# Kernel tuning notes

Measured on AMD Instinct MI355X. Metric: run time of the kernel, lower is better.

The kernel has to match this reference:

```python
import jax, jax.numpy as jnp
import numpy as np

B, L, E, D, A = 32, 2048, 1024, 1024, 1024

def setup_inputs() -> dict:
    key = jax.random.key(0)
    k1, k2, k3, k4, k5 = jax.random.split(key, 5)
    s_e = 1.0 / np.sqrt(E)
    s_d = 1.0 / np.sqrt(D)
    s_a = 1.0 / np.sqrt(A)
    return {
        "encoder_outputs": jax.random.normal(k1, (B, L, E), dtype=jnp.float32),
        "decoder_hidden": jax.random.normal(k2, (B, D), dtype=jnp.float32),
        "mask": jnp.ones((B, L), dtype=jnp.int32),
        # nn.Linear weights are [out, in]; uniform(-1/sqrt(in), 1/sqrt(in))
        "W1": jax.random.uniform(k3, (A, E), jnp.float32, -s_e, s_e),
        "W2": jax.random.uniform(k4, (A, D), jnp.float32, -s_d, s_d),
        "v": jax.random.uniform(k5, (1, A), jnp.float32, -s_a, s_a),
    }

def reference(encoder_outputs, decoder_hidden, mask, W1, W2, v):
    # enc_t: [B,L,A], dec_t: [B,1,A]
    enc_t = jnp.einsum('ble,ae->bla', encoder_outputs, W1)
    dec_t = jnp.einsum('bd,ad->ba', decoder_hidden, W2)[:, None, :]
    combined = jnp.tanh(enc_t + dec_t)                       # [B,L,A]
    scores = jnp.einsum('bla,a->bl', combined, v[0])          # [B,L]
    scores = jnp.where(mask == 0, -jnp.inf, scores)
    attn = jax.nn.softmax(scores, axis=-1)                    # [B,L]
    context = jnp.einsum('bl,ble->be', attn, encoder_outputs) # [B,E]
    return (context, attn)
```

## Files before the change

kernel.cpp:

```cpp
#include <hip/hip_runtime.h>
#include <stdint.h>

typedef __bf16 bf16x8 __attribute__((ext_vector_type(8)));
typedef float f32x4 __attribute__((ext_vector_type(4)));
typedef unsigned short ushort8v __attribute__((ext_vector_type(8)));

__device__ __forceinline__ void gload_lds16(const void* g, void* l) {
  __builtin_amdgcn_global_load_lds(
      (const __attribute__((address_space(1))) void*)g,
      (__attribute__((address_space(3))) void*)l, 16, 0, 0);
}

__device__ __forceinline__ unsigned short f2bf(float f) {
  union { float f; unsigned int u; } x; x.f = f;
  unsigned int r = x.u + 0x7FFFu + ((x.u >> 16) & 1u);
  return (unsigned short)(r >> 16);
}

__device__ __forceinline__ float ftanh(float x) {
  float ax = fabsf(x);
  float e = __expf(-2.0f * ax);
  float r = (1.0f - e) / (1.0f + e);
  return copysignf(r, x);
}

__global__ __launch_bounds__(256) void w1cvt_kernel(
    const float* __restrict__ W1, unsigned short* __restrict__ w1b) {
  const int g = blockIdx.x * 256 + threadIdx.x;
  const int chunk = g >> 9;
  const int dpos = (g & 511) * 16;
  const int ntile = chunk >> 5, kstep = chunk & 31;
  const int col = dpos >> 6;
  const int k0 = (dpos & 63) >> 1;
  const float* src = W1 + (size_t)(ntile * 128 + col) * 1024 + kstep * 32 + k0;
  const float4 v0 = *(const float4*)src;
  const float4 v1 = *(const float4*)(src + 4);
  ushort8v o;
  o[0] = f2bf(v0.x); o[1] = f2bf(v0.y); o[2] = f2bf(v0.z); o[3] = f2bf(v0.w);
  o[4] = f2bf(v1.x); o[5] = f2bf(v1.y); o[6] = f2bf(v1.z); o[7] = f2bf(v1.w);
  *((ushort8v*)w1b + g) = o;
}

__global__ __launch_bounds__(256) void dec_proj_kernel(
    const float* __restrict__ dec, const float* __restrict__ W2,
    float* __restrict__ u) {
  __shared__ __align__(16) float w2s[1024];
  const int a = blockIdx.x;
  const int t = threadIdx.x;
  *(float4*)(w2s + t * 4) = *(const float4*)(W2 + (size_t)a * 1024 + t * 4);
  __syncthreads();
  const int wid = t >> 6, l = t & 63;
  for (int bi = 0; bi < 8; ++bi) {
    const int b = wid * 8 + bi;
    const float* dp = dec + (size_t)b * 1024;
    float acc = 0.f;
#pragma unroll
    for (int i = 0; i < 4; ++i) {
      const int k = i * 256 + l * 4;
      const float4 dv = *(const float4*)(dp + k);
      const float4 wv = *(const float4*)(w2s + k);
      acc = fmaf(dv.x, wv.x, acc); acc = fmaf(dv.y, wv.y, acc);
      acc = fmaf(dv.z, wv.z, acc); acc = fmaf(dv.w, wv.w, acc);
    }
#pragma unroll
    for (int m = 1; m < 64; m <<= 1) acc += __shfl_xor(acc, m, 64);
    if (l == 0) u[(size_t)b * 1024 + a] = acc;
  }
}

__global__ __launch_bounds__(256, 3) void scores_kernel(
    const float* __restrict__ enc, const unsigned short* __restrict__ w1b,
    const float* __restrict__ u, const float* __restrict__ vvec,
    float* __restrict__ spart) {
  __shared__ __align__(16) char Al[16384];
  __shared__ __align__(16) char Bl[16384];
  __shared__ __align__(16) float sred[256];

  const int t = threadIdx.x;
  const int bid = blockIdx.x;
  const int panel = (bid & 7) + ((bid >> 6) << 3);
  const int ntile = (bid >> 3) & 7;
  const int m0 = panel * 128;
  const int n0 = ntile * 128;
  const int b = panel >> 4;
  const int l = t & 63, wid = t >> 6;
  const int wr = wid >> 1, wc = wid & 1;
  const int lm = l & 15, lg = l >> 4;

  const char* w1c = (const char*)w1b + (size_t)ntile * 262144;
  const float* ub = u + (size_t)b * 1024;

  const int abase = (wr * 64 + lm) * 64 + lg * 16;
  const int bbase = (wc * 64 + lm) * 64 + lg * 16;

  const int arow0 = t >> 2;
  const int ak0 = (t & 3) * 8;
  const float* encA = enc + (size_t)(m0 + arow0) * 1024 + ak0;
  const float* encB = enc + (size_t)(m0 + 64 + arow0) * 1024 + ak0;
  const int adst = t * 16;

  f32x4 acc[4][4];
#pragma unroll
  for (int mi = 0; mi < 4; ++mi)
#pragma unroll
    for (int ni = 0; ni < 4; ++ni) acc[mi][ni] = (f32x4){0.f, 0.f, 0.f, 0.f};

  gload_lds16(w1c + t * 16, Bl + t * 16);
  gload_lds16(w1c + 4096 + t * 16, Bl + 4096 + t * 16);
  {
    const float4 p0 = *(const float4*)encA;
    const float4 p1 = *(const float4*)(encA + 4);
    const float4 p2 = *(const float4*)encB;
    const float4 p3 = *(const float4*)(encB + 4);
    ushort8v o0, o1;
    o0[0] = f2bf(p0.x); o0[1] = f2bf(p0.y); o0[2] = f2bf(p0.z); o0[3] = f2bf(p0.w);
    o0[4] = f2bf(p1.x); o0[5] = f2bf(p1.y); o0[6] = f2bf(p1.z); o0[7] = f2bf(p1.w);
    o1[0] = f2bf(p2.x); o1[1] = f2bf(p2.y); o1[2] = f2bf(p2.z); o1[3] = f2bf(p2.w);
    o1[4] = f2bf(p3.x); o1[5] = f2bf(p3.y); o1[6] = f2bf(p3.z); o1[7] = f2bf(p3.w);
    *(ushort8v*)(Al + adst) = o0;
    *(ushort8v*)(Al + 4096 + adst) = o1;
  }
  __syncthreads();

#pragma unroll 2
  for (int ks = 0; ks < 32; ++ks) {
    const int buf = (ks & 1) * 8192;
    const int nbuf = buf ^ 8192;
    float4 p0, p1, p2, p3;
    if (ks < 31) {
      const char* wnext = w1c + (size_t)(ks + 1) * 8192;
      gload_lds16(wnext + t * 16, Bl + nbuf + t * 16);
      gload_lds16(wnext + 4096 + t * 16, Bl + nbuf + 4096 + t * 16);
      const float* ea = encA + (ks + 1) * 32;
      const float* eb = encB + (ks + 1) * 32;
      p0 = *(const float4*)ea;
      p1 = *(const float4*)(ea + 4);
      p2 = *(const float4*)eb;
      p3 = *(const float4*)(eb + 4);
    }
    bf16x8 af[4], bf[4];
#pragma unroll
    for (int mi = 0; mi < 4; ++mi)
      af[mi] = *(const bf16x8*)(Al + buf + abase + mi * 1024);
#pragma unroll
    for (int ni = 0; ni < 4; ++ni)
      bf[ni] = *(const bf16x8*)(Bl + buf + bbase + ni * 1024);
    __builtin_amdgcn_s_setprio(1);
#pragma unroll
    for (int mi = 0; mi < 4; ++mi)
#pragma unroll
      for (int ni = 0; ni < 4; ++ni)
        acc[mi][ni] = __builtin_amdgcn_mfma_f32_16x16x32_bf16(
            af[mi], bf[ni], acc[mi][ni], 0, 0, 0);
    __builtin_amdgcn_s_setprio(0);
    if (ks < 31) {
      ushort8v o0, o1;
      o0[0] = f2bf(p0.x); o0[1] = f2bf(p0.y); o0[2] = f2bf(p0.z); o0[3] = f2bf(p0.w);
      o0[4] = f2bf(p1.x); o0[5] = f2bf(p1.y); o0[6] = f2bf(p1.z); o0[7] = f2bf(p1.w);
      o1[0] = f2bf(p2.x); o1[1] = f2bf(p2.y); o1[2] = f2bf(p2.z); o1[3] = f2bf(p2.w);
      o1[4] = f2bf(p3.x); o1[5] = f2bf(p3.y); o1[6] = f2bf(p3.z); o1[7] = f2bf(p3.w);
      *(ushort8v*)(Al + nbuf + adst) = o0;
      *(ushort8v*)(Al + nbuf + 4096 + adst) = o1;
    }
    __syncthreads();
  }

  float rowp[4][4];
#pragma unroll
  for (int mi = 0; mi < 4; ++mi)
#pragma unroll
    for (int j = 0; j < 4; ++j) rowp[mi][j] = 0.f;
#pragma unroll
  for (int ni = 0; ni < 4; ++ni) {
    const int colA = n0 + wc * 64 + ni * 16 + lm;
    const float uu = ub[colA], vv = vvec[colA];
#pragma unroll
    for (int mi = 0; mi < 4; ++mi)
#pragma unroll
      for (int j = 0; j < 4; ++j)
        rowp[mi][j] += ftanh(acc[mi][ni][j] + uu) * vv;
  }
#pragma unroll
  for (int m = 1; m < 16; m <<= 1)
#pragma unroll
    for (int mi = 0; mi < 4; ++mi)
#pragma unroll
      for (int j = 0; j < 4; ++j) rowp[mi][j] += __shfl_xor(rowp[mi][j], m, 64);
  if (lm == 0) {
#pragma unroll
    for (int mi = 0; mi < 4; ++mi)
#pragma unroll
      for (int j = 0; j < 4; ++j)
        sred[wc * 128 + wr * 64 + mi * 16 + lg * 4 + j] = rowp[mi][j];
  }
  __syncthreads();
  if (t < 128) {
    spart[(size_t)ntile * 65536 + m0 + t] = sred[t] + sred[128 + t];
  }
}

__global__ __launch_bounds__(256) void softmax_kernel(
    const float* __restrict__ spart, float* __restrict__ out,
    const int* __restrict__ mask) {
  __shared__ float wred[4];
  const int bidx = blockIdx.x;
  const int t = threadIdx.x;
  const int r8 = bidx * 2048 + t * 8;
  float* at = out + 32768 + (size_t)bidx * 2048;
  const int* mk = mask + (size_t)bidx * 2048;
  float v[8] = {0.f, 0.f, 0.f, 0.f, 0.f, 0.f, 0.f, 0.f};
#pragma unroll
  for (int nt = 0; nt < 8; ++nt) {
    const float4 s0 = *(const float4*)(spart + (size_t)nt * 65536 + r8);
    const float4 s1 = *(const float4*)(spart + (size_t)nt * 65536 + r8 + 4);
    v[0] += s0.x; v[1] += s0.y; v[2] += s0.z; v[3] += s0.w;
    v[4] += s1.x; v[5] += s1.y; v[6] += s1.z; v[7] += s1.w;
  }
  const int4 q0 = *(const int4*)(mk + t * 8);
  const int4 q1 = *(const int4*)(mk + t * 8 + 4);
  int q[8] = {q0.x, q0.y, q0.z, q0.w, q1.x, q1.y, q1.z, q1.w};
  float mx = -3.0e38f;
#pragma unroll
  for (int j = 0; j < 8; ++j) if (q[j] != 0) mx = fmaxf(mx, v[j]);
#pragma unroll
  for (int m = 1; m < 64; m <<= 1) mx = fmaxf(mx, __shfl_xor(mx, m, 64));
  if ((t & 63) == 0) wred[t >> 6] = mx;
  __syncthreads();
  mx = fmaxf(fmaxf(wred[0], wred[1]), fmaxf(wred[2], wred[3]));
  __syncthreads();
  float pp[8]; float sum = 0.f;
#pragma unroll
  for (int j = 0; j < 8; ++j) {
    pp[j] = (q[j] != 0) ? __expf(v[j] - mx) : 0.f;
    sum += pp[j];
  }
#pragma unroll
  for (int m = 1; m < 64; m <<= 1) sum += __shfl_xor(sum, m, 64);
  if ((t & 63) == 0) wred[t >> 6] = sum;
  __syncthreads();
  sum = (wred[0] + wred[1]) + (wred[2] + wred[3]);
  const float inv = 1.0f / sum;
  const float4 o0 = {pp[0] * inv, pp[1] * inv, pp[2] * inv, pp[3] * inv};
  const float4 o1 = {pp[4] * inv, pp[5] * inv, pp[6] * inv, pp[7] * inv};
  *(float4*)(at + t * 8) = o0;
  *(float4*)(at + t * 8 + 4) = o1;
}

__global__ __launch_bounds__(256) void context_kernel(
    const float* __restrict__ enc, float* __restrict__ out) {
  __shared__ __align__(16) float attnS[2048];
  __shared__ __align__(16) float red[8 * 128];
  const int bid = blockIdx.x;
  const int b = bid >> 3, ec = bid & 7;
  const int e0 = ec * 128;
  const int t = threadIdx.x;
  const float* attn = out + 32768 + (size_t)b * 2048;
#pragma unroll
  for (int i = 0; i < 8; ++i) attnS[i * 256 + t] = attn[i * 256 + t];
  __syncthreads();
  const int el = (t & 31) * 4;
  const int ls = t >> 5;
  f32x4 acc = {0.f, 0.f, 0.f, 0.f};
  const float* ebase = enc + (size_t)b * 2048 * 1024 + e0 + el;
  for (int l2 = ls; l2 < 2048; l2 += 8) {
    const float a = attnS[l2];
    const float4 ev = *(const float4*)(ebase + (size_t)l2 * 1024);
    acc[0] = fmaf(a, ev.x, acc[0]);
    acc[1] = fmaf(a, ev.y, acc[1]);
    acc[2] = fmaf(a, ev.z, acc[2]);
    acc[3] = fmaf(a, ev.w, acc[3]);
  }
  *(f32x4*)(red + ls * 128 + el) = acc;
  __syncthreads();
  if (t < 128) {
    float s = 0.f;
#pragma unroll
    for (int i = 0; i < 8; ++i) s += red[i * 128 + t];
    out[(size_t)b * 1024 + e0 + t] = s;
  }
}

extern "C" void kernel_launch(void* const* d_in, const int* in_sizes, int n_in,
                              void* d_out, int out_size, void* d_ws,
                              size_t ws_size, hipStream_t stream) {
  const float* enc = (const float*)d_in[0];
  const float* dec = (const float*)d_in[1];
  const int* mask = (const int*)d_in[2];
  const float* W1 = (const float*)d_in[3];
  const float* W2 = (const float*)d_in[4];
  const float* v = (const float*)d_in[5];
  float* out = (float*)d_out;
  char* ws = (char*)d_ws;
  unsigned short* w1b = (unsigned short*)ws;
  float* u = (float*)(ws + (2u << 20));
  float* spart = (float*)(ws + (2u << 20) + (128u << 10));

  w1cvt_kernel<<<512, 256, 0, stream>>>(W1, w1b);
  dec_proj_kernel<<<1024, 256, 0, stream>>>(dec, W2, u);
  scores_kernel<<<4096, 256, 0, stream>>>(enc, w1b, u, v, spart);
  softmax_kernel<<<32, 256, 0, stream>>>(spart, out, mask);
  context_kernel<<<256, 256, 0, stream>>>(enc, out);
}
```

Measured before the change: 324.2 us.

## Widen scores GEMM tile to 128x256 and XOR-swizzle LDS layout

```diff
diff --git a/kernel.cpp b/kernel.cpp
--- a/kernel.cpp
+++ b/kernel.cpp
@@ -27,12 +27,12 @@
 __global__ __launch_bounds__(256) void w1cvt_kernel(
     const float* __restrict__ W1, unsigned short* __restrict__ w1b) {
   const int g = blockIdx.x * 256 + threadIdx.x;
-  const int chunk = g >> 9;
-  const int dpos = (g & 511) * 16;
-  const int ntile = chunk >> 5, kstep = chunk & 31;
-  const int col = dpos >> 6;
-  const int k0 = (dpos & 63) >> 1;
-  const float* src = W1 + (size_t)(ntile * 128 + col) * 1024 + kstep * 32 + k0;
+  const int chunk = g >> 10;
+  const int d16 = g & 1023;
+  const int col = d16 >> 2, s = d16 & 3;
+  const int np = chunk >> 5, ks = chunk & 31;
+  const float* src = W1 + (size_t)(np * 256 + col) * 1024 + ks * 32 +
+                     ((s ^ ((col >> 1) & 3)) * 8);
   const float4 v0 = *(const float4*)src;
   const float4 v1 = *(const float4*)(src + 4);
   ushort8v o;
@@ -68,50 +68,51 @@
   }
 }
 
-__global__ __launch_bounds__(256, 3) void scores_kernel(
+__global__ __launch_bounds__(256, 2) void scores_kernel(
     const float* __restrict__ enc, const unsigned short* __restrict__ w1b,
     const float* __restrict__ u, const float* __restrict__ vvec,
     float* __restrict__ spart) {
   __shared__ __align__(16) char Al[16384];
-  __shared__ __align__(16) char Bl[16384];
+  __shared__ __align__(16) char Bl[32768];
   __shared__ __align__(16) float sred[256];
 
   const int t = threadIdx.x;
   const int bid = blockIdx.x;
-  const int panel = (bid & 7) + ((bid >> 6) << 3);
-  const int ntile = (bid >> 3) & 7;
+  const int np = (bid >> 3) & 3;
+  const int panel = (bid & 7) + ((bid >> 5) << 3);
   const int m0 = panel * 128;
-  const int n0 = ntile * 128;
+  const int n0 = np * 256;
   const int b = panel >> 4;
   const int l = t & 63, wid = t >> 6;
   const int wr = wid >> 1, wc = wid & 1;
   const int lm = l & 15, lg = l >> 4;
 
-  const char* w1c = (const char*)w1b + (size_t)ntile * 262144;
+  const int soff = (lg ^ ((lm >> 1) & 3)) * 16;
+  const int abase = (wr * 64 + lm) * 64 + soff;
+  const int bbase = (wc * 128 + lm) * 64 + soff;
+  const char* w1base = (const char*)w1b + (size_t)(np * 32) * 16384;
   const float* ub = u + (size_t)b * 1024;
 
-  const int abase = (wr * 64 + lm) * 64 + lg * 16;
-  const int bbase = (wc * 64 + lm) * 64 + lg * 16;
-
-  const int arow0 = t >> 2;
-  const int ak0 = (t & 3) * 8;
-  const float* encA = enc + (size_t)(m0 + arow0) * 1024 + ak0;
-  const float* encB = enc + (size_t)(m0 + 64 + arow0) * 1024 + ak0;
+  const int row0 = t >> 2;
+  const int s0 = t & 3;
+  const int xo = (s0 ^ ((row0 >> 1) & 3)) * 8;
+  const float* srcA = enc + (size_t)(m0 + row0) * 1024 + xo;
   const int adst = t * 16;
 
-  f32x4 acc[4][4];
+  f32x4 acc[4][8];
 #pragma unroll
   for (int mi = 0; mi < 4; ++mi)
 #pragma unroll
-    for (int ni = 0; ni < 4; ++ni) acc[mi][ni] = (f32x4){0.f, 0.f, 0.f, 0.f};
-
-  gload_lds16(w1c + t * 16, Bl + t * 16);
-  gload_lds16(w1c + 4096 + t * 16, Bl + 4096 + t * 16);
+    for (int ni = 0; ni < 8; ++ni) acc[mi][ni] = (f32x4){0.f, 0.f, 0.f, 0.f};
+
+#pragma unroll
+  for (int i = 0; i < 4; ++i)
+    gload_lds16(w1base + i * 4096 + t * 16, Bl + i * 4096 + t * 16);
   {
-    const float4 p0 = *(const float4*)encA;
-    const float4 p1 = *(const float4*)(encA + 4);
-    const float4 p2 = *(const float4*)encB;
-    const float4 p3 = *(const float4*)(encB + 4);
+    const float4 p0 = *(const float4*)srcA;
+    const float4 p1 = *(const float4*)(srcA + 4);
+    const float4 p2 = *(const float4*)(srcA + 65536);
+    const float4 p3 = *(const float4*)(srcA + 65540);
     ushort8v o0, o1;
     o0[0] = f2bf(p0.x); o0[1] = f2bf(p0.y); o0[2] = f2bf(p0.z); o0[3] = f2bf(p0.w);
     o0[4] = f2bf(p1.x); o0[5] = f2bf(p1.y); o0[6] = f2bf(p1.z); o0[7] = f2bf(p1.w);
@@ -124,32 +125,33 @@
 
 #pragma unroll 2
   for (int ks = 0; ks < 32; ++ks) {
-    const int buf = (ks & 1) * 8192;
-    const int nbuf = buf ^ 8192;
+    const int abuf = (ks & 1) * 8192;
+    const int bbuf = (ks & 1) * 16384;
     float4 p0, p1, p2, p3;
     if (ks < 31) {
-      const char* wnext = w1c + (size_t)(ks + 1) * 8192;
-      gload_lds16(wnext + t * 16, Bl + nbuf + t * 16);
-      gload_lds16(wnext + 4096 + t * 16, Bl + nbuf + 4096 + t * 16);
-      const float* ea = encA + (ks + 1) * 32;
-      const float* eb = encB + (ks + 1) * 32;
-      p0 = *(const float4*)ea;
-      p1 = *(const float4*)(ea + 4);
-      p2 = *(const float4*)eb;
-      p3 = *(const float4*)(eb + 4);
+      const char* wn = w1base + (size_t)(ks + 1) * 16384;
+#pragma unroll
+      for (int i = 0; i < 4; ++i)
+        gload_lds16(wn + i * 4096 + t * 16,
+                    Bl + (bbuf ^ 16384) + i * 4096 + t * 16);
+      const float* sa = srcA + (ks + 1) * 32;
+      p0 = *(const float4*)sa;
+      p1 = *(const float4*)(sa + 4);
+      p2 = *(const float4*)(sa + 65536);
+      p3 = *(const float4*)(sa + 65540);
     }
-    bf16x8 af[4], bf[4];
-#pragma unroll
-    for (int mi = 0; mi < 4; ++mi)
-      af[mi] = *(const bf16x8*)(Al + buf + abase + mi * 1024);
-#pragma unroll
-    for (int ni = 0; ni < 4; ++ni)
-      bf[ni] = *(const bf16x8*)(Bl + buf + bbase + ni * 1024);
+    bf16x8 af[4], bf[8];
+#pragma unroll
+    for (int mi = 0; mi < 4; ++mi)
+      af[mi] = *(const bf16x8*)(Al + abuf + abase + mi * 1024);
+#pragma unroll
+    for (int ni = 0; ni < 8; ++ni)
+      bf[ni] = *(const bf16x8*)(Bl + bbuf + bbase + ni * 1024);
     __builtin_amdgcn_s_setprio(1);
 #pragma unroll
     for (int mi = 0; mi < 4; ++mi)
 #pragma unroll
-      for (int ni = 0; ni < 4; ++ni)
+      for (int ni = 0; ni < 8; ++ni)
         acc[mi][ni] = __builtin_amdgcn_mfma_f32_16x16x32_bf16(
             af[mi], bf[ni], acc[mi][ni], 0, 0, 0);
     __builtin_amdgcn_s_setprio(0);
@@ -159,8 +161,8 @@
       o0[4] = f2bf(p1.x); o0[5] = f2bf(p1.y); o0[6] = f2bf(p1.z); o0[7] = f2bf(p1.w);
       o1[0] = f2bf(p2.x); o1[1] = f2bf(p2.y); o1[2] = f2bf(p2.z); o1[3] = f2bf(p2.w);
       o1[4] = f2bf(p3.x); o1[5] = f2bf(p3.y); o1[6] = f2bf(p3.z); o1[7] = f2bf(p3.w);
-      *(ushort8v*)(Al + nbuf + adst) = o0;
-      *(ushort8v*)(Al + nbuf + 4096 + adst) = o1;
+      *(ushort8v*)(Al + (abuf ^ 8192) + adst) = o0;
+      *(ushort8v*)(Al + (abuf ^ 8192) + 4096 + adst) = o1;
     }
     __syncthreads();
   }
@@ -171,8 +173,8 @@
 #pragma unroll
     for (int j = 0; j < 4; ++j) rowp[mi][j] = 0.f;
 #pragma unroll
-  for (int ni = 0; ni < 4; ++ni) {
-    const int colA = n0 + wc * 64 + ni * 16 + lm;
+  for (int ni = 0; ni < 8; ++ni) {
+    const int colA = n0 + wc * 128 + ni * 16 + lm;
     const float uu = ub[colA], vv = vvec[colA];
 #pragma unroll
     for (int mi = 0; mi < 4; ++mi)
@@ -195,7 +197,7 @@
   }
   __syncthreads();
   if (t < 128) {
-    spart[(size_t)ntile * 65536 + m0 + t] = sred[t] + sred[128 + t];
+    spart[(size_t)np * 65536 + m0 + t] = sred[t] + sred[128 + t];
   }
 }
 
@@ -210,9 +212,9 @@
   const int* mk = mask + (size_t)bidx * 2048;
   float v[8] = {0.f, 0.f, 0.f, 0.f, 0.f, 0.f, 0.f, 0.f};
 #pragma unroll
-  for (int nt = 0; nt < 8; ++nt) {
-    const float4 s0 = *(const float4*)(spart + (size_t)nt * 65536 + r8);
-    const float4 s1 = *(const float4*)(spart + (size_t)nt * 65536 + r8 + 4);
+  for (int np = 0; np < 4; ++np) {
+    const float4 s0 = *(const float4*)(spart + (size_t)np * 65536 + r8);
+    const float4 s1 = *(const float4*)(spart + (size_t)np * 65536 + r8 + 4);
     v[0] += s0.x; v[1] += s0.y; v[2] += s0.z; v[3] += s0.w;
     v[4] += s1.x; v[5] += s1.y; v[6] += s1.z; v[7] += s1.w;
   }
@@ -297,7 +299,7 @@
 
   w1cvt_kernel<<<512, 256, 0, stream>>>(W1, w1b);
   dec_proj_kernel<<<1024, 256, 0, stream>>>(dec, W2, u);
-  scores_kernel<<<4096, 256, 0, stream>>>(enc, w1b, u, v, spart);
+  scores_kernel<<<2048, 256, 0, stream>>>(enc, w1b, u, v, spart);
   softmax_kernel<<<32, 256, 0, stream>>>(spart, out, mask);
   context_kernel<<<256, 256, 0, stream>>>(enc, out);
 }
```

Measured after the change: 275.0 us. 15.2% less time.
